# Performance work log

Hardware: AMD Instinct MI355X
Metric: run time of the kernel (lower is better)

## Reference

```python
import jax, jax.numpy as jnp
import numpy as np

B, S, D_MODEL = 2, 2048, 1024
N_HEADS, D_HEAD = 16, 64
ATTN_SCALE = float(np.sqrt(D_HEAD))
IGNORE = -100000.0


def setup_inputs() -> dict:
    key = jax.random.key(0)
    ks = jax.random.split(key, 8)
    scale = 1.0 / np.sqrt(D_MODEL)
    return {
        "x": jax.random.normal(ks[0], (B, S, D_MODEL), jnp.float32),
        "pos_embed": jax.random.normal(ks[1], (B, S, D_MODEL), jnp.float32),
        "W_Q": jax.random.normal(ks[2], (N_HEADS, D_MODEL, D_HEAD), jnp.float32) * scale,
        "b_Q": jnp.zeros((N_HEADS, D_HEAD), jnp.float32),
        "W_K": jax.random.normal(ks[3], (N_HEADS, D_MODEL, D_HEAD), jnp.float32) * scale,
        "b_K": jnp.zeros((N_HEADS, D_HEAD), jnp.float32),
        "W_V": jax.random.normal(ks[4], (N_HEADS, D_MODEL, D_HEAD), jnp.float32) * scale,
        "b_V": jnp.zeros((N_HEADS, D_HEAD), jnp.float32),
        "W_O": jax.random.normal(ks[5], (N_HEADS, D_HEAD, D_MODEL), jnp.float32) * (1.0 / np.sqrt(D_HEAD)),
        "b_O": jnp.zeros((D_MODEL,), jnp.float32),
    }


def reference(x, pos_embed, W_Q, b_Q, W_K, b_K, W_V, b_V, W_O, b_O):
    # use_pos_resid=False: q,k read x+pos_embed, v reads x
    attn_input = x + pos_embed                                   # [b,p,m]
    q = jnp.einsum('bpm,imh->bpih', attn_input, W_Q) + b_Q       # [b,p,i,h]
    k = jnp.einsum('bpm,imh->bpih', attn_input, W_K) + b_K
    v = jnp.einsum('bpm,imh->bpih', x, W_V) + b_V
    # scores[b,i,p,q]: query index p attends to key index q
    scores = jnp.einsum('bpih,bqih->bipq', q, k) / ATTN_SCALE
    S_len = scores.shape[-1]
    causal = jnp.tril(jnp.ones((S_len, S_len), bool))
    scores = jnp.where(causal, scores, IGNORE)
    attn = jax.nn.softmax(scores, axis=-1)                       # [b,i,q_dst,p_src]
    z = jnp.einsum('bpih,biqp->bqih', v, attn)                   # [b,q,i,h]
    out = jnp.einsum('bqih,ihm->bqm', z, W_O) + b_O              # [b,q,m]
    return out
```

## Files before the change

### kernel.cpp

```cpp
#include <hip/hip_runtime.h>
#include <hip/hip_bf16.h>
#include <stdint.h>

typedef __hip_bfloat16 bf16;
typedef __attribute__((ext_vector_type(8))) short short8;
typedef __attribute__((ext_vector_type(4))) short short4v;
typedef __attribute__((ext_vector_type(4))) float f32x4;
typedef __attribute__((ext_vector_type(16))) float f32x16;
typedef __attribute__((ext_vector_type(4))) unsigned uint4v;
typedef __attribute__((ext_vector_type(2))) unsigned uint2v;

#define AS1 __attribute__((address_space(1)))
#define AS3 __attribute__((address_space(3)))

static constexpr int SEQ = 2048, DM = 1024, DHD = 64;
static constexpr int MROWS = 2 * SEQ;

__device__ __forceinline__ short f2b(float f) {
  __hip_bfloat16 h = __float2bfloat16(f);
  return *reinterpret_cast<short*>(&h);
}

__device__ __forceinline__ unsigned pack2(float lo, float hi) {
  float2 fv; fv.x = lo; fv.y = hi;
  union { __hip_bfloat162 h; unsigned u; } cv;
  cv.h = __float22bfloat162_rn(fv);
  return cv.u;
}

__device__ __forceinline__ float fexp2(float x) {
#if __has_builtin(__builtin_amdgcn_exp2f)
  return __builtin_amdgcn_exp2f(x);
#else
  return exp2f(x);
#endif
}

union U8 { uint4v u; short8 s; };

#define GL16(dst, ptr, off) \
  asm volatile("global_load_dwordx4 %0, %1, off offset:" #off : "=v"(dst) : "v"(ptr))
#define WAITV(n) do { asm volatile("s_waitcnt vmcnt(" #n ")"); __builtin_amdgcn_sched_barrier(0); } while (0)

__device__ __forceinline__ float xmax32(float v) {
#if __has_builtin(__builtin_amdgcn_permlane32_swap)
  uint2v r = __builtin_amdgcn_permlane32_swap(__float_as_uint(v), __float_as_uint(v), false, false);
  return fmaxf(__uint_as_float(r[0]), __uint_as_float(r[1]));
#else
  return fmaxf(v, __shfl_xor(v, 32));
#endif
}
__device__ __forceinline__ float xsum32(float v) {
#if __has_builtin(__builtin_amdgcn_permlane32_swap)
  uint2v r = __builtin_amdgcn_permlane32_swap(__float_as_uint(v), __float_as_uint(v), false, false);
  return __uint_as_float(r[0]) + __uint_as_float(r[1]);
#else
  return v + __shfl_xor(v, 32);
#endif
}

__global__ __launch_bounds__(256) void preprocess(const float* __restrict__ x,
                                                  const float* __restrict__ pos,
                                                  bf16* __restrict__ xb,
                                                  bf16* __restrict__ aib,
                                                  const float* __restrict__ wq,
                                                  const float* __restrict__ wk,
                                                  const float* __restrict__ wv,
                                                  const float* __restrict__ wo,
                                                  bf16* __restrict__ oq,
                                                  bf16* __restrict__ ok,
                                                  bf16* __restrict__ ov,
                                                  bf16* __restrict__ owo) {
  const int bid = blockIdx.x;
  if (bid < 4096) {
    int i = bid * 256 + threadIdx.x;
    f32x4 xv = ((const f32x4*)x)[i];
    f32x4 pv = ((const f32x4*)pos)[i];
    short4v xo, ao;
#pragma unroll
    for (int j = 0; j < 4; ++j) {
      xo[j] = f2b(xv[j]);
      ao[j] = f2b(xv[j] + pv[j]);
    }
    ((short4v*)xb)[i] = xo;
    ((short4v*)aib)[i] = ao;
    return;
  }
  __shared__ float t[64][65];
  const float* in;
  bf16* out;
  int C, rt, ct;
  if (bid < 4864) {
    int idx = bid - 4096;
    int z = idx >> 4;
    rt = idx & 15; ct = 0; C = 64;
    const float* w = (z < 16) ? wq : (z < 32) ? wk : wv;
    bf16* o = (z < 16) ? oq : (z < 32) ? ok : ov;
    int zz = z & 15;
    in = w + (size_t)zz * 1024 * 64;
    out = o + (size_t)zz * 1024 * 64;
  } else {
    int idx = bid - 4864;
    ct = idx & 15; rt = idx >> 4; C = 1024;
    in = wo; out = owo;
  }
  int c = threadIdx.x & 63, g = threadIdx.x >> 6;
#pragma unroll
  for (int j = 0; j < 16; ++j) {
    int r = g * 16 + j;
    t[r][c] = in[(size_t)(rt * 64 + r) * C + (ct * 64 + c)];
  }
  __syncthreads();
#pragma unroll
  for (int j = 0; j < 16; ++j) {
    int rr = g * 16 + j;
    out[(size_t)(ct * 64 + rr) * 1024 + (rt * 64 + c)] = __float2bfloat16(t[c][rr]);
  }
}

template <int MODE>
__device__ __forceinline__ void gemm128_body(const bf16* __restrict__ A,
                                             const bf16* __restrict__ Bt,
                                             const float* __restrict__ bias,
                                             bf16* __restrict__ C, int mt, int nt,
                                             float scale) {
  __shared__ alignas(16) bf16 Al[128 * 32];
  __shared__ alignas(16) bf16 Bl[128 * 32];
  const int lane = threadIdx.x & 63, wv = threadIdx.x >> 6;
  const int wr = wv >> 1, wc = wv & 1;
  const bf16* Ab = A + (size_t)mt * 128 * DM;
  const bf16* Bb = Bt + (size_t)nt * 128 * DM;

  f32x4 acc[4][4];
#pragma unroll
  for (int i = 0; i < 4; ++i)
#pragma unroll
    for (int j = 0; j < 4; ++j) acc[i][j] = (f32x4){0.f, 0.f, 0.f, 0.f};

  for (int kt = 0; kt < DM / 32; ++kt) {
    int k0 = kt * 32;
#pragma unroll
    for (int c = 0; c < 2; ++c) {
      int li0 = wv * 64 + c * 256;
      int li = li0 + lane;
      int row = li >> 2, sl = li & 3;
      int gs = sl ^ ((row >> 1) & 3);
      __builtin_amdgcn_global_load_lds((const AS1 void*)(Ab + (size_t)row * DM + k0 + gs * 8),
                                       (AS3 void*)(&Al[li0 * 8]), 16, 0, 0);
    }
#pragma unroll
    for (int c = 0; c < 2; ++c) {
      int li0 = wv * 64 + c * 256;
      int li = li0 + lane;
      int row = li >> 2, sl = li & 3;
      int gs = sl ^ ((row >> 1) & 3);
      __builtin_amdgcn_global_load_lds((const AS1 void*)(Bb + (size_t)row * DM + k0 + gs * 8),
                                       (AS3 void*)(&Bl[li0 * 8]), 16, 0, 0);
    }
    __syncthreads();

    short8 af[4], bfr[4];
    const int kb = lane >> 4;
#pragma unroll
    for (int mi = 0; mi < 4; ++mi) {
      int r = wr * 64 + mi * 16 + (lane & 15);
      af[mi] = *(const short8*)(&Al[r * 32 + ((kb ^ ((r >> 1) & 3)) << 3)]);
    }
#pragma unroll
    for (int ni = 0; ni < 4; ++ni) {
      int r = wc * 64 + ni * 16 + (lane & 15);
      bfr[ni] = *(const short8*)(&Bl[r * 32 + ((kb ^ ((r >> 1) & 3)) << 3)]);
    }
#pragma unroll
    for (int mi = 0; mi < 4; ++mi)
#pragma unroll
      for (int ni = 0; ni < 4; ++ni)
        acc[mi][ni] = __builtin_amdgcn_mfma_f32_16x16x32_bf16(af[mi], bfr[ni], acc[mi][ni], 0, 0, 0);
    __syncthreads();
  }

#pragma unroll
  for (int mi = 0; mi < 4; ++mi) {
#pragma unroll
    for (int ni = 0; ni < 4; ++ni) {
      int row0 = mt * 128 + wr * 64 + mi * 16 + (lane >> 4) * 4;
      int col = nt * 128 + wc * 64 + ni * 16 + (lane & 15);
      float bv = bias[col];
      int bb = row0 >> 11, s0 = row0 & 2047;
      int hh = col >> 6, d0 = col & 63;
      size_t bhb = (size_t)(bb * 16 + hh) * 131072;
      if constexpr (MODE == 3) {
        int kc = d0 >> 4, hi = (d0 >> 3) & 1, e = d0 & 7;
        int g = s0 >> 5, r0 = s0 & 31;
        size_t bbase = bhb + g * 2048 + kc * 512 + e;
#pragma unroll
        for (int j = 0; j < 4; ++j)
          C[bbase + (size_t)(r0 + j + 32 * hi) * 8] =
              __float2bfloat16((acc[mi][ni][j] + bv) * scale);
      } else {
        int dj = d0 >> 5, d32 = d0 & 31;
        int ks = s0 >> 4, hi2 = (s0 >> 3) & 1, e0 = s0 & 7;
        short4v o;
#pragma unroll
        for (int j = 0; j < 4; ++j) o[j] = f2b(acc[mi][ni][j] + bv);
        *(short4v*)(C + bhb + dj * 65536 + ks * 512 + (size_t)(d32 + 32 * hi2) * 8 + e0) = o;
      }
    }
  }
}

static constexpr float QSCALE = 0.125f * 1.4426950408889634f;

__global__ __launch_bounds__(256) void qkv_gemm(const bf16* __restrict__ aib,
                                                const bf16* __restrict__ xb,
                                                const bf16* __restrict__ wqt,
                                                const bf16* __restrict__ wkt,
                                                const bf16* __restrict__ wvt,
                                                const float* __restrict__ bq,
                                                const float* __restrict__ bk,
                                                const float* __restrict__ bv,
                                                bf16* __restrict__ FQ, bf16* __restrict__ FK,
                                                bf16* __restrict__ FV) {
  int mt = blockIdx.x & 31;
  int nt = (blockIdx.x >> 5) & 7;
  int mat = blockIdx.x >> 8;
  if (mat == 0) {
    gemm128_body<3>(aib, wqt, bq, FQ, mt, nt, QSCALE);
  } else if (mat == 1) {
    gemm128_body<3>(aib, wkt, bk, FK, mt, nt, 1.0f);
  } else {
    gemm128_body<4>(xb, wvt, bv, FV, mt, nt, 1.0f);
  }
}

__global__ __launch_bounds__(256) void o_gemm64(const bf16* __restrict__ A,
                                                const bf16* __restrict__ Bt,
                                                const float* __restrict__ bias,
                                                float* __restrict__ out) {
  __shared__ alignas(16) bf16 Al[64 * 128];
  __shared__ alignas(16) bf16 Bl[128 * 128];
  const int mt = blockIdx.x & 63, nt = blockIdx.x >> 6;
  const int lane = threadIdx.x & 63, wv = threadIdx.x >> 6;
  const int wr = wv >> 1, wc = wv & 1;
  const bf16* Ab = A + (size_t)mt * 64 * DM;
  const bf16* Bb = Bt + (size_t)nt * 128 * DM;

  f32x4 acc[2][4];
#pragma unroll
  for (int i = 0; i < 2; ++i)
#pragma unroll
    for (int j = 0; j < 4; ++j) acc[i][j] = (f32x4){0.f, 0.f, 0.f, 0.f};

  for (int kt = 0; kt < DM / 128; ++kt) {
    int k0 = kt * 128;
#pragma unroll
    for (int c = 0; c < 4; ++c) {
      int li0 = wv * 64 + c * 256;
      int li = li0 + lane;
      int row = li >> 4, sl = li & 15;
      int gs = sl ^ (row & 7);
      __builtin_amdgcn_global_load_lds((const AS1 void*)(Ab + (size_t)row * DM + k0 + gs * 8),
                                       (AS3 void*)(&Al[li0 * 8]), 16, 0, 0);
    }
#pragma unroll
    for (int c = 0; c < 8; ++c) {
      int li0 = wv * 64 + c * 256;
      int li = li0 + lane;
      int row = li >> 4, sl = li & 15;
      int gs = sl ^ (row & 7);
      __builtin_amdgcn_global_load_lds((const AS1 void*)(Bb + (size_t)row * DM + k0 + gs * 8),
                                       (AS3 void*)(&Bl[li0 * 8]), 16, 0, 0);
    }
    __syncthreads();

    const int kb = lane >> 4;
#pragma unroll
    for (int kk = 0; kk < 4; ++kk) {
      short8 af[2], bfr[4];
#pragma unroll
      for (int mi = 0; mi < 2; ++mi) {
        int r = wr * 32 + mi * 16 + (lane & 15);
        af[mi] = *(const short8*)(&Al[r * 128 + (((kb + 4 * kk) ^ (r & 7)) << 3)]);
      }
#pragma unroll
      for (int ni = 0; ni < 4; ++ni) {
        int r = wc * 64 + ni * 16 + (lane & 15);
        bfr[ni] = *(const short8*)(&Bl[r * 128 + (((kb + 4 * kk) ^ (r & 7)) << 3)]);
      }
#pragma unroll
      for (int mi = 0; mi < 2; ++mi)
#pragma unroll
        for (int ni = 0; ni < 4; ++ni)
          acc[mi][ni] = __builtin_amdgcn_mfma_f32_16x16x32_bf16(af[mi], bfr[ni], acc[mi][ni], 0, 0, 0);
    }
    __syncthreads();
  }

#pragma unroll
  for (int mi = 0; mi < 2; ++mi) {
#pragma unroll
    for (int ni = 0; ni < 4; ++ni) {
      int row0 = mt * 64 + wr * 32 + mi * 16 + (lane >> 4) * 4;
      int col = nt * 128 + wc * 64 + ni * 16 + (lane & 15);
      float bv = bias[col];
#pragma unroll
      for (int j = 0; j < 4; ++j)
        out[(size_t)(row0 + j) * DM + col] = acc[mi][ni][j] + bv;
    }
  }
}

__global__ __launch_bounds__(128, 2) void flash_attn(const bf16* __restrict__ FQ,
                                                     const bf16* __restrict__ FK,
                                                     const bf16* __restrict__ FV,
                                                     bf16* __restrict__ Zb) {
  __shared__ float Zm[64][33];
  __shared__ float Ml[64], Ll[64];
  __shared__ unsigned Zl[32 * 32];

  const int lane = threadIdx.x & 63;
  const int wvi = threadIdx.x >> 6;
  const int qln = lane & 31;
  const bool hib = lane >= 32;
  const int bh = blockIdx.x & 31;
  const int wq = 63 - (blockIdx.x >> 5);
  const int bb = bh >> 4, h = bh & 15;
  const int q0 = wq * 32;
  const int nt = wq / 2 + 1;
  const int hsp = (nt + 1) >> 1;
  const int t0 = wvi ? hsp : 0;
  const int t1 = wvi ? nt : hsp;

  const size_t fb = (size_t)bh * 131072;
  const bf16* qp = FQ + fb + wq * 2048 + lane * 8;
  const bf16* kpt = FK + fb + (size_t)t0 * 4096 + lane * 8;
  const bf16* vp0 = FV + fb + (size_t)t0 * 2048 + lane * 8;
  const bf16* vp1 = vp0 + 65536;

  f32x16 zacc[2];
#pragma unroll
  for (int i = 0; i < 16; ++i) { zacc[0][i] = 0.f; zacc[1][i] = 0.f; }
  float mrun = -1e30f, lrun = 0.f;

  short8 qf[4];
  short8 kfA[2][4], kfB[2][4];
  short8 vf[2][4];

  if (t0 < t1) {
    GL16(qf[0], qp, 0); GL16(qf[1], qp, 1024); GL16(qf[2], qp, 2048); GL16(qf[3], qp, 3072);
    {
      const bf16* k1 = kpt + 2048;
      GL16(kfA[0][0], kpt, 0); GL16(kfA[0][1], kpt, 1024); GL16(kfA[0][2], kpt, 2048); GL16(kfA[0][3], kpt, 3072);
      GL16(kfA[1][0], k1, 0);  GL16(kfA[1][1], k1, 1024);  GL16(kfA[1][2], k1, 2048);  GL16(kfA[1][3], k1, 3072);
      kpt += 4096;
    }
    GL16(vf[0][0], vp0, 0); GL16(vf[0][1], vp0, 1024); GL16(vf[0][2], vp0, 2048); GL16(vf[0][3], vp0, 3072);
    GL16(vf[1][0], vp1, 0); GL16(vf[1][1], vp1, 1024); GL16(vf[1][2], vp1, 2048); GL16(vf[1][3], vp1, 3072);
    vp0 += 2048; vp1 += 2048;

    auto computeT = [&](short8(&kf)[2][4], short8(&kfn)[2][4], int t) {
      const int kv0 = t * 64;
      const bool pref = (t + 1 < t1);

      WAITV(8);

      f32x16 s[2];
#pragma unroll
      for (int i = 0; i < 16; ++i) { s[0][i] = 0.f; s[1][i] = 0.f; }
      __builtin_amdgcn_s_setprio(1);
#pragma unroll
      for (int kc = 0; kc < 4; ++kc) {
        s[0] = __builtin_amdgcn_mfma_f32_32x32x16_bf16(kf[0][kc], qf[kc], s[0], 0, 0, 0);
        s[1] = __builtin_amdgcn_mfma_f32_32x32x16_bf16(kf[1][kc], qf[kc], s[1], 0, 0, 0);
      }
      __builtin_amdgcn_s_setprio(0);

      if (pref) {
        const bf16* k1 = kpt + 2048;
        GL16(kfn[0][0], kpt, 0); GL16(kfn[0][1], kpt, 1024); GL16(kfn[0][2], kpt, 2048); GL16(kfn[0][3], kpt, 3072);
        GL16(kfn[1][0], k1, 0);  GL16(kfn[1][1], k1, 1024);  GL16(kfn[1][2], k1, 2048);  GL16(kfn[1][3], k1, 3072);
        kpt += 4096;
      }

      if (t == nt - 1) {
        const int qg = q0 + qln;
#pragma unroll
        for (int ni = 0; ni < 2; ++ni)
#pragma unroll
          for (int rr = 0; rr < 16; ++rr) {
            int kv = kv0 + 32 * ni + (rr & 3) + 8 * (rr >> 2) + (hib ? 4 : 0);
            if (kv > qg) s[ni][rr] = -1e30f;
          }
      }

      float t8[8];
#pragma unroll
      for (int i = 0; i < 8; ++i)
        t8[i] = fmaxf(fmaxf(s[0][i], s[0][i + 8]), fmaxf(s[1][i], s[1][i + 8]));
      float tm = fmaxf(fmaxf(fmaxf(t8[0], t8[1]), fmaxf(t8[2], t8[3])),
                       fmaxf(fmaxf(t8[4], t8[5]), fmaxf(t8[6], t8[7])));
      tm = xmax32(tm);

      if (__ballot(tm > mrun + 8.0f)) {
        float mn = fmaxf(mrun, tm);
        float al = fexp2(mrun - mn);
        mrun = mn;
        lrun *= al;
#pragma unroll
        for (int i = 0; i < 16; ++i) { zacc[0][i] *= al; zacc[1][i] *= al; }
      }

      float pacc[4] = {0.f, 0.f, 0.f, 0.f};
#pragma unroll
      for (int ni = 0; ni < 2; ++ni)
#pragma unroll
        for (int rr = 0; rr < 16; ++rr) {
          float p = fexp2(s[ni][rr] - mrun);
          s[ni][rr] = p;
          pacc[rr & 3] += p;
        }
      lrun += xsum32((pacc[0] + pacc[1]) + (pacc[2] + pacc[3]));

      unsigned su32[2][8];
#pragma unroll
      for (int ni = 0; ni < 2; ++ni)
#pragma unroll
        for (int tt = 0; tt < 8; ++tt)
          su32[ni][tt] = pack2(s[ni][2 * tt], s[ni][2 * tt + 1]);

      short8 pa[4];
#if __has_builtin(__builtin_amdgcn_permlane32_swap)
#pragma unroll
      for (int c = 0; c < 4; ++c) {
        int ni = c >> 1, b4 = 4 * (c & 1);
        uint2v r0 = __builtin_amdgcn_permlane32_swap(su32[ni][b4 + 0], su32[ni][b4 + 2], false, false);
        uint2v r1 = __builtin_amdgcn_permlane32_swap(su32[ni][b4 + 1], su32[ni][b4 + 3], false, false);
        U8 w;
        w.u[0] = r0[0]; w.u[1] = r1[0]; w.u[2] = r0[1]; w.u[3] = r1[1];
        pa[c] = w.s;
      }
#else
      unsigned X[2][8];
#pragma unroll
      for (int ni = 0; ni < 2; ++ni)
#pragma unroll
        for (int tt = 0; tt < 8; ++tt)
          X[ni][tt] = (unsigned)__shfl_xor((int)su32[ni][tt], 32);
#pragma unroll
      for (int c = 0; c < 4; ++c) {
        int ni = c >> 1, b4 = 4 * (c & 1);
        U8 w;
        w.u[0] = hib ? X[ni][b4 + 2] : su32[ni][b4 + 0];
        w.u[1] = hib ? X[ni][b4 + 3] : su32[ni][b4 + 1];
        w.u[2] = hib ? su32[ni][b4 + 2] : X[ni][b4 + 0];
        w.u[3] = hib ? su32[ni][b4 + 3] : X[ni][b4 + 1];
        pa[c] = w.s;
      }
#endif

      if (pref) { WAITV(8); } else { WAITV(0); }

      __builtin_amdgcn_s_setprio(1);
#pragma unroll
      for (int c = 0; c < 4; ++c) {
        zacc[0] = __builtin_amdgcn_mfma_f32_32x32x16_bf16(vf[0][c], pa[c], zacc[0], 0, 0, 0);
        zacc[1] = __builtin_amdgcn_mfma_f32_32x32x16_bf16(vf[1][c], pa[c], zacc[1], 0, 0, 0);
      }
      __builtin_amdgcn_s_setprio(0);
      __builtin_amdgcn_sched_barrier(0);

      if (pref) {
        GL16(vf[0][0], vp0, 0); GL16(vf[0][1], vp0, 1024); GL16(vf[0][2], vp0, 2048); GL16(vf[0][3], vp0, 3072);
        GL16(vf[1][0], vp1, 0); GL16(vf[1][1], vp1, 1024); GL16(vf[1][2], vp1, 2048); GL16(vf[1][3], vp1, 3072);
        vp0 += 2048; vp1 += 2048;
      }
    };

    int t = t0;
    while (true) {
      computeT(kfA, kfB, t);
      if (++t >= t1) break;
      computeT(kfB, kfA, t);
      if (++t >= t1) break;
    }
  }

  if (wvi == 1) {
#pragma unroll
    for (int i = 0; i < 16; ++i) {
      Zm[lane][i] = zacc[0][i];
      Zm[lane][16 + i] = zacc[1][i];
    }
    Ml[lane] = mrun;
    Ll[lane] = lrun;
  }
  __syncthreads();
  if (wvi == 0) {
    float m1 = Ml[lane], l1 = Ll[lane];
    float mn = fmaxf(mrun, m1);
    float a0 = fexp2(mrun - mn);
    float a1 = fexp2(m1 - mn);
    float lm = lrun * a0 + l1 * a1;
#pragma unroll
    for (int i = 0; i < 16; ++i) {
      zacc[0][i] = zacc[0][i] * a0 + Zm[lane][i] * a1;
      zacc[1][i] = zacc[1][i] * a0 + Zm[lane][16 + i] * a1;
    }

    const float rl = 1.0f / lm;
    const int W8[8] = {0, 1, 4, 5, 8, 9, 12, 13};
#pragma unroll
    for (int dj = 0; dj < 2; ++dj)
#pragma unroll
      for (int tt = 0; tt < 8; ++tt) {
        unsigned v = pack2(zacc[dj][2 * tt] * rl, zacc[dj][2 * tt + 1] * rl);
        int x = 16 * dj + (hib ? 2 : 0) + W8[tt];
        Zl[qln * 32 + (((x >> 2) ^ (qln & 7)) << 2) + (x & 3)] = v;
      }
    asm volatile("s_waitcnt lgkmcnt(0)" ::: "memory");
    __builtin_amdgcn_sched_barrier(0);
    const size_t base = ((size_t)bb * SEQ) * DM + h * DHD;
    int q2 = lane >> 1, hf = lane & 1;
#pragma unroll
    for (int u = 0; u < 4; ++u) {
      int sl = (hf * 4 + u) ^ (q2 & 7);
      U8 w;
      w.u = *(const uint4v*)&Zl[q2 * 32 + sl * 4];
      *(short8*)(Zb + base + (size_t)(q0 + q2) * DM + hf * 32 + u * 8) = w.s;
    }
  }
}

extern "C" void kernel_launch(void* const* d_in, const int* in_sizes, int n_in,
                              void* d_out, int out_size, void* d_ws, size_t ws_size,
                              hipStream_t stream) {
  (void)in_sizes; (void)n_in; (void)out_size; (void)ws_size;
  const float* x = (const float*)d_in[0];
  const float* pos = (const float*)d_in[1];
  const float* WQ = (const float*)d_in[2];
  const float* bQ = (const float*)d_in[3];
  const float* WK = (const float*)d_in[4];
  const float* bK = (const float*)d_in[5];
  const float* WV = (const float*)d_in[6];
  const float* bV = (const float*)d_in[7];
  const float* WO = (const float*)d_in[8];
  const float* bO = (const float*)d_in[9];
  float* out = (float*)d_out;

  bf16* ws = (bf16*)d_ws;
  size_t off = 0;
  bf16* aib = ws + off; off += (size_t)MROWS * DM;
  bf16* xb  = ws + off; off += (size_t)MROWS * DM;
  bf16* wqt = ws + off; off += (size_t)DM * DM;
  bf16* wkt = ws + off; off += (size_t)DM * DM;
  bf16* wvt = ws + off; off += (size_t)DM * DM;
  bf16* wot = ws + off; off += (size_t)DM * DM;
  bf16* FQ  = ws + off; off += (size_t)MROWS * DM;
  bf16* FK  = ws + off; off += (size_t)MROWS * DM;
  bf16* FV  = ws + off; off += (size_t)MROWS * DM;
  bf16* Zb  = ws + off; off += (size_t)MROWS * DM;

  preprocess<<<5120, 256, 0, stream>>>(x, pos, xb, aib, WQ, WK, WV, WO,
                                       wqt, wkt, wvt, wot);
  qkv_gemm<<<768, 256, 0, stream>>>(aib, xb, wqt, wkt, wvt, bQ, bK, bV, FQ, FK, FV);
  flash_attn<<<2048, 128, 0, stream>>>(FQ, FK, FV, Zb);
  o_gemm64<<<512, 256, 0, stream>>>(Zb, wot, bO, out);
}
```

Baseline: 103.6 us.

## Pair long and short causal query tiles per block to balance attention work

Each flash-attention block now handles two query tiles, a long one (63-p) and a short one (p), instead of one. The work of both is split between the two waves: wave 0 runs the first part of the long tile, and wave 1 runs the rest of the long tile followed by the whole short tile. The long tile's two partial softmax states are merged through shared memory, and each wave writes out one tile. This halves the grid and evens out causal-triangle work across blocks, meant to cut tail imbalance. The cost is fewer blocks for latency hiding and serial segments inside wave 1.

```diff
diff --git a/kernel.cpp b/kernel.cpp
--- a/kernel.cpp
+++ b/kernel.cpp
@@ -316,37 +316,155 @@
                                                      bf16* __restrict__ Zb) {
   __shared__ float Zm[64][33];
   __shared__ float Ml[64], Ll[64];
-  __shared__ unsigned Zl[32 * 32];
+  __shared__ unsigned Zl[2][32 * 32];
 
   const int lane = threadIdx.x & 63;
   const int wvi = threadIdx.x >> 6;
   const int qln = lane & 31;
   const bool hib = lane >= 32;
   const int bh = blockIdx.x & 31;
-  const int wq = 63 - (blockIdx.x >> 5);
-  const int bb = bh >> 4, h = bh & 15;
-  const int q0 = wq * 32;
-  const int nt = wq / 2 + 1;
-  const int hsp = (nt + 1) >> 1;
-  const int t0 = wvi ? hsp : 0;
-  const int t1 = wvi ? nt : hsp;
-
+  const int p = blockIdx.x >> 5;
+  const int wqA = 63 - p, wqB = p;
+  const int nA = wqA / 2 + 1, nB = wqB / 2 + 1;
+  int h = (nA + nB + 1) >> 1;
+  if (h > nA) h = nA;
+  const int bb = bh >> 4, hd = bh & 15;
   const size_t fb = (size_t)bh * 131072;
-  const bf16* qp = FQ + fb + wq * 2048 + lane * 8;
-  const bf16* kpt = FK + fb + (size_t)t0 * 4096 + lane * 8;
-  const bf16* vp0 = FV + fb + (size_t)t0 * 2048 + lane * 8;
-  const bf16* vp1 = vp0 + 65536;
+  const size_t base = ((size_t)bb * SEQ) * DM + hd * DHD;
 
   f32x16 zacc[2];
-#pragma unroll
-  for (int i = 0; i < 16; ++i) { zacc[0][i] = 0.f; zacc[1][i] = 0.f; }
-  float mrun = -1e30f, lrun = 0.f;
-
+  float mrun, lrun;
   short8 qf[4];
   short8 kfA[2][4], kfB[2][4];
   short8 vf[2][4];
 
-  if (t0 < t1) {
+  auto computeT = [&](short8(&kf)[2][4], short8(&kfn)[2][4], int t, int q0,
+                      int ntq, int te, const bf16*& kpt, const bf16*& vp0,
+                      const bf16*& vp1) {
+    const int kv0 = t * 64;
+    const bool pref = (t + 1 < te);
+
+    WAITV(8);
+
+    f32x16 s[2];
+#pragma unroll
+    for (int i = 0; i < 16; ++i) { s[0][i] = 0.f; s[1][i] = 0.f; }
+    __builtin_amdgcn_s_setprio(1);
+#pragma unroll
+    for (int kc = 0; kc < 4; ++kc) {
+      s[0] = __builtin_amdgcn_mfma_f32_32x32x16_bf16(kf[0][kc], qf[kc], s[0], 0, 0, 0);
+      s[1] = __builtin_amdgcn_mfma_f32_32x32x16_bf16(kf[1][kc], qf[kc], s[1], 0, 0, 0);
+    }
+    __builtin_amdgcn_s_setprio(0);
+
+    if (pref) {
+      const bf16* k1 = kpt + 2048;
+      GL16(kfn[0][0], kpt, 0); GL16(kfn[0][1], kpt, 1024); GL16(kfn[0][2], kpt, 2048); GL16(kfn[0][3], kpt, 3072);
+      GL16(kfn[1][0], k1, 0);  GL16(kfn[1][1], k1, 1024);  GL16(kfn[1][2], k1, 2048);  GL16(kfn[1][3], k1, 3072);
+      kpt += 4096;
+    }
+
+    if (t == ntq - 1) {
+      const int qg = q0 + qln;
+#pragma unroll
+      for (int ni = 0; ni < 2; ++ni)
+#pragma unroll
+        for (int rr = 0; rr < 16; ++rr) {
+          int kv = kv0 + 32 * ni + (rr & 3) + 8 * (rr >> 2) + (hib ? 4 : 0);
+          if (kv > qg) s[ni][rr] = -1e30f;
+        }
+    }
+
+    float t8[8];
+#pragma unroll
+    for (int i = 0; i < 8; ++i)
+      t8[i] = fmaxf(fmaxf(s[0][i], s[0][i + 8]), fmaxf(s[1][i], s[1][i + 8]));
+    float tm = fmaxf(fmaxf(fmaxf(t8[0], t8[1]), fmaxf(t8[2], t8[3])),
+                     fmaxf(fmaxf(t8[4], t8[5]), fmaxf(t8[6], t8[7])));
+    tm = xmax32(tm);
+
+    if (__ballot(tm > mrun + 8.0f)) {
+      float mn = fmaxf(mrun, tm);
+      float al = fexp2(mrun - mn);
+      mrun = mn;
+      lrun *= al;
+#pragma unroll
+      for (int i = 0; i < 16; ++i) { zacc[0][i] *= al; zacc[1][i] *= al; }
+    }
+
+    float pacc[4] = {0.f, 0.f, 0.f, 0.f};
+#pragma unroll
+    for (int ni = 0; ni < 2; ++ni)
+#pragma unroll
+      for (int rr = 0; rr < 16; ++rr) {
+        float pw = fexp2(s[ni][rr] - mrun);
+        s[ni][rr] = pw;
+        pacc[rr & 3] += pw;
+      }
+    lrun += xsum32((pacc[0] + pacc[1]) + (pacc[2] + pacc[3]));
+
+    unsigned su32[2][8];
+#pragma unroll
+    for (int ni = 0; ni < 2; ++ni)
+#pragma unroll
+      for (int tt = 0; tt < 8; ++tt)
+        su32[ni][tt] = pack2(s[ni][2 * tt], s[ni][2 * tt + 1]);
+
+    short8 pa[4];
+#if __has_builtin(__builtin_amdgcn_permlane32_swap)
+#pragma unroll
+    for (int c = 0; c < 4; ++c) {
+      int ni = c >> 1, b4 = 4 * (c & 1);
+      uint2v r0 = __builtin_amdgcn_permlane32_swap(su32[ni][b4 + 0], su32[ni][b4 + 2], false, false);
+      uint2v r1 = __builtin_amdgcn_permlane32_swap(su32[ni][b4 + 1], su32[ni][b4 + 3], false, false);
+      U8 w;
+      w.u[0] = r0[0]; w.u[1] = r1[0]; w.u[2] = r0[1]; w.u[3] = r1[1];
+      pa[c] = w.s;
+    }
+#else
+    unsigned X[2][8];
+#pragma unroll
+    for (int ni = 0; ni < 2; ++ni)
+#pragma unroll
+      for (int tt = 0; tt < 8; ++tt)
+        X[ni][tt] = (unsigned)__shfl_xor((int)su32[ni][tt], 32);
+#pragma unroll
+    for (int c = 0; c < 4; ++c) {
+      int ni = c >> 1, b4 = 4 * (c & 1);
+      U8 w;
+      w.u[0] = hib ? X[ni][b4 + 2] : su32[ni][b4 + 0];
+      w.u[1] = hib ? X[ni][b4 + 3] : su32[ni][b4 + 1];
+      w.u[2] = hib ? su32[ni][b4 + 2] : X[ni][b4 + 0];
+      w.u[3] = hib ? su32[ni][b4 + 3] : X[ni][b4 + 1];
+      pa[c] = w.s;
+    }
+#endif
+
+    if (pref) { WAITV(8); } else { WAITV(0); }
+
+    __builtin_amdgcn_s_setprio(1);
+#pragma unroll
+    for (int c = 0; c < 4; ++c) {
+      zacc[0] = __builtin_amdgcn_mfma_f32_32x32x16_bf16(vf[0][c], pa[c], zacc[0], 0, 0, 0);
+      zacc[1] = __builtin_amdgcn_mfma_f32_32x32x16_bf16(vf[1][c], pa[c], zacc[1], 0, 0, 0);
+    }
+    __builtin_amdgcn_s_setprio(0);
+    __builtin_amdgcn_sched_barrier(0);
+
+    if (pref) {
+      GL16(vf[0][0], vp0, 0); GL16(vf[0][1], vp0, 1024); GL16(vf[0][2], vp0, 2048); GL16(vf[0][3], vp0, 3072);
+      GL16(vf[1][0], vp1, 0); GL16(vf[1][1], vp1, 1024); GL16(vf[1][2], vp1, 2048); GL16(vf[1][3], vp1, 3072);
+      vp0 += 2048; vp1 += 2048;
+    }
+  };
+
+  auto runSeg = [&](int qt, int ntq, int ts, int te) {
+    if (ts >= te) return;
+    const int q0 = qt * 32;
+    const bf16* qp = FQ + fb + qt * 2048 + lane * 8;
+    const bf16* kpt = FK + fb + (size_t)ts * 4096 + lane * 8;
+    const bf16* vp0 = FV + fb + (size_t)ts * 2048 + lane * 8;
+    const bf16* vp1 = vp0 + 65536;
     GL16(qf[0], qp, 0); GL16(qf[1], qp, 1024); GL16(qf[2], qp, 2048); GL16(qf[3], qp, 3072);
     {
       const bf16* k1 = kpt + 2048;
@@ -358,134 +476,50 @@
     GL16(vf[1][0], vp1, 0); GL16(vf[1][1], vp1, 1024); GL16(vf[1][2], vp1, 2048); GL16(vf[1][3], vp1, 3072);
     vp0 += 2048; vp1 += 2048;
 
-    auto computeT = [&](short8(&kf)[2][4], short8(&kfn)[2][4], int t) {
-      const int kv0 = t * 64;
-      const bool pref = (t + 1 < t1);
-
-      WAITV(8);
-
-      f32x16 s[2];
-#pragma unroll
-      for (int i = 0; i < 16; ++i) { s[0][i] = 0.f; s[1][i] = 0.f; }
-      __builtin_amdgcn_s_setprio(1);
-#pragma unroll
-      for (int kc = 0; kc < 4; ++kc) {
-        s[0] = __builtin_amdgcn_mfma_f32_32x32x16_bf16(kf[0][kc], qf[kc], s[0], 0, 0, 0);
-        s[1] = __builtin_amdgcn_mfma_f32_32x32x16_bf16(kf[1][kc], qf[kc], s[1], 0, 0, 0);
+    int t = ts;
+    while (true) {
+      computeT(kfA, kfB, t, q0, ntq, te, kpt, vp0, vp1);
+      if (++t >= te) break;
+      computeT(kfB, kfA, t, q0, ntq, te, kpt, vp0, vp1);
+      if (++t >= te) break;
+    }
+  };
+
+  auto resetState = [&]() {
+#pragma unroll
+    for (int i = 0; i < 16; ++i) { zacc[0][i] = 0.f; zacc[1][i] = 0.f; }
+    mrun = -1e30f; lrun = 0.f;
+  };
+
+  auto writeOut = [&](int qt, float lm, unsigned* Zbuf) {
+    const float rl = 1.0f / lm;
+    const int W8[8] = {0, 1, 4, 5, 8, 9, 12, 13};
+#pragma unroll
+    for (int dj = 0; dj < 2; ++dj)
+#pragma unroll
+      for (int tt = 0; tt < 8; ++tt) {
+        unsigned v = pack2(zacc[dj][2 * tt] * rl, zacc[dj][2 * tt + 1] * rl);
+        int x = 16 * dj + (hib ? 2 : 0) + W8[tt];
+        Zbuf[qln * 32 + (((x >> 2) ^ (qln & 7)) << 2) + (x & 3)] = v;
       }
-      __builtin_amdgcn_s_setprio(0);
-
-      if (pref) {
-        const bf16* k1 = kpt + 2048;
-        GL16(kfn[0][0], kpt, 0); GL16(kfn[0][1], kpt, 1024); GL16(kfn[0][2], kpt, 2048); GL16(kfn[0][3], kpt, 3072);
-        GL16(kfn[1][0], k1, 0);  GL16(kfn[1][1], k1, 1024);  GL16(kfn[1][2], k1, 2048);  GL16(kfn[1][3], k1, 3072);
-        kpt += 4096;
-      }
-
-      if (t == nt - 1) {
-        const int qg = q0 + qln;
-#pragma unroll
-        for (int ni = 0; ni < 2; ++ni)
-#pragma unroll
-          for (int rr = 0; rr < 16; ++rr) {
-            int kv = kv0 + 32 * ni + (rr & 3) + 8 * (rr >> 2) + (hib ? 4 : 0);
-            if (kv > qg) s[ni][rr] = -1e30f;
-          }
-      }
-
-      float t8[8];
-#pragma unroll
-      for (int i = 0; i < 8; ++i)
-        t8[i] = fmaxf(fmaxf(s[0][i], s[0][i + 8]), fmaxf(s[1][i], s[1][i + 8]));
-      float tm = fmaxf(fmaxf(fmaxf(t8[0], t8[1]), fmaxf(t8[2], t8[3])),
-                       fmaxf(fmaxf(t8[4], t8[5]), fmaxf(t8[6], t8[7])));
-      tm = xmax32(tm);
-
-      if (__ballot(tm > mrun + 8.0f)) {
-        float mn = fmaxf(mrun, tm);
-        float al = fexp2(mrun - mn);
-        mrun = mn;
-        lrun *= al;
-#pragma unroll
-        for (int i = 0; i < 16; ++i) { zacc[0][i] *= al; zacc[1][i] *= al; }
-      }
-
-      float pacc[4] = {0.f, 0.f, 0.f, 0.f};
-#pragma unroll
-      for (int ni = 0; ni < 2; ++ni)
-#pragma unroll
-        for (int rr = 0; rr < 16; ++rr) {
-          float p = fexp2(s[ni][rr] - mrun);
-          s[ni][rr] = p;
-          pacc[rr & 3] += p;
-        }
-      lrun += xsum32((pacc[0] + pacc[1]) + (pacc[2] + pacc[3]));
-
-      unsigned su32[2][8];
-#pragma unroll
-      for (int ni = 0; ni < 2; ++ni)
-#pragma unroll
-        for (int tt = 0; tt < 8; ++tt)
-          su32[ni][tt] = pack2(s[ni][2 * tt], s[ni][2 * tt + 1]);
-
-      short8 pa[4];
-#if __has_builtin(__builtin_amdgcn_permlane32_swap)
-#pragma unroll
-      for (int c = 0; c < 4; ++c) {
-        int ni = c >> 1, b4 = 4 * (c & 1);
-        uint2v r0 = __builtin_amdgcn_permlane32_swap(su32[ni][b4 + 0], su32[ni][b4 + 2], false, false);
-        uint2v r1 = __builtin_amdgcn_permlane32_swap(su32[ni][b4 + 1], su32[ni][b4 + 3], false, false);
-        U8 w;
-        w.u[0] = r0[0]; w.u[1] = r1[0]; w.u[2] = r0[1]; w.u[3] = r1[1];
-        pa[c] = w.s;
-      }
-#else
-      unsigned X[2][8];
-#pragma unroll
-      for (int ni = 0; ni < 2; ++ni)
-#pragma unroll
-        for (int tt = 0; tt < 8; ++tt)
-          X[ni][tt] = (unsigned)__shfl_xor((int)su32[ni][tt], 32);
-#pragma unroll
-      for (int c = 0; c < 4; ++c) {
-        int ni = c >> 1, b4 = 4 * (c & 1);
-        U8 w;
-        w.u[0] = hib ? X[ni][b4 + 2] : su32[ni][b4 + 0];
-        w.u[1] = hib ? X[ni][b4 + 3] : su32[ni][b4 + 1];
-        w.u[2] = hib ? su32[ni][b4 + 2] : X[ni][b4 + 0];
-        w.u[3] = hib ? su32[ni][b4 + 3] : X[ni][b4 + 1];
-        pa[c] = w.s;
-      }
-#endif
-
-      if (pref) { WAITV(8); } else { WAITV(0); }
-
-      __builtin_amdgcn_s_setprio(1);
-#pragma unroll
-      for (int c = 0; c < 4; ++c) {
-        zacc[0] = __builtin_amdgcn_mfma_f32_32x32x16_bf16(vf[0][c], pa[c], zacc[0], 0, 0, 0);
-        zacc[1] = __builtin_amdgcn_mfma_f32_32x32x16_bf16(vf[1][c], pa[c], zacc[1], 0, 0, 0);
-      }
-      __builtin_amdgcn_s_setprio(0);
-      __builtin_amdgcn_sched_barrier(0);
-
-      if (pref) {
-        GL16(vf[0][0], vp0, 0); GL16(vf[0][1], vp0, 1024); GL16(vf[0][2], vp0, 2048); GL16(vf[0][3], vp0, 3072);
-        GL16(vf[1][0], vp1, 0); GL16(vf[1][1], vp1, 1024); GL16(vf[1][2], vp1, 2048); GL16(vf[1][3], vp1, 3072);
-        vp0 += 2048; vp1 += 2048;
-      }
-    };
-
-    int t = t0;
-    while (true) {
-      computeT(kfA, kfB, t);
-      if (++t >= t1) break;
-      computeT(kfB, kfA, t);
-      if (++t >= t1) break;
-    }
-  }
-
-  if (wvi == 1) {
+    asm volatile("s_waitcnt lgkmcnt(0)" ::: "memory");
+    __builtin_amdgcn_sched_barrier(0);
+    int q2 = lane >> 1, hf = lane & 1;
+#pragma unroll
+    for (int u = 0; u < 4; ++u) {
+      int sl = (hf * 4 + u) ^ (q2 & 7);
+      U8 w;
+      w.u = *(const uint4v*)&Zbuf[q2 * 32 + sl * 4];
+      *(short8*)(Zb + base + (size_t)(qt * 32 + q2) * DM + hf * 32 + u * 8) = w.s;
+    }
+  };
+
+  if (wvi == 0) {
+    resetState();
+    runSeg(wqA, nA, 0, h);
+  } else {
+    resetState();
+    runSeg(wqA, nA, h, nA);
 #pragma unroll
     for (int i = 0; i < 16; ++i) {
       Zm[lane][i] = zacc[0][i];
@@ -493,8 +527,11 @@
     }
     Ml[lane] = mrun;
     Ll[lane] = lrun;
+    resetState();
+    runSeg(wqB, nB, 0, nB);
   }
   __syncthreads();
+
   if (wvi == 0) {
     float m1 = Ml[lane], l1 = Ll[lane];
     float mn = fmaxf(mrun, m1);
@@ -506,28 +543,9 @@
       zacc[0][i] = zacc[0][i] * a0 + Zm[lane][i] * a1;
       zacc[1][i] = zacc[1][i] * a0 + Zm[lane][16 + i] * a1;
     }
-
-    const float rl = 1.0f / lm;
-    const int W8[8] = {0, 1, 4, 5, 8, 9, 12, 13};
-#pragma unroll
-    for (int dj = 0; dj < 2; ++dj)
-#pragma unroll
-      for (int tt = 0; tt < 8; ++tt) {
-        unsigned v = pack2(zacc[dj][2 * tt] * rl, zacc[dj][2 * tt + 1] * rl);
-        int x = 16 * dj + (hib ? 2 : 0) + W8[tt];
-        Zl[qln * 32 + (((x >> 2) ^ (qln & 7)) << 2) + (x & 3)] = v;
-      }
-    asm volatile("s_waitcnt lgkmcnt(0)" ::: "memory");
-    __builtin_amdgcn_sched_barrier(0);
-    const size_t base = ((size_t)bb * SEQ) * DM + h * DHD;
-    int q2 = lane >> 1, hf = lane & 1;
-#pragma unroll
-    for (int u = 0; u < 4; ++u) {
-      int sl = (hf * 4 + u) ^ (q2 & 7);
-      U8 w;
-      w.u = *(const uint4v*)&Zl[q2 * 32 + sl * 4];
-      *(short8*)(Zb + base + (size_t)(q0 + q2) * DM + hf * 32 + u * 8) = w.s;
-    }
+    writeOut(wqA, lm, Zl[0]);
+  } else {
+    writeOut(wqB, lrun, Zl[1]);
   }
 }
 
@@ -563,6 +581,6 @@
   preprocess<<<5120, 256, 0, stream>>>(x, pos, xb, aib, WQ, WK, WV, WO,
                                        wqt, wkt, wvt, wot);
   qkv_gemm<<<768, 256, 0, stream>>>(aib, xb, wqt, wkt, wvt, bQ, bK, bV, FQ, FK, FV);
-  flash_attn<<<2048, 128, 0, stream>>>(FQ, FK, FV, Zb);
+  flash_attn<<<1024, 128, 0, stream>>>(FQ, FK, FV, Zb);
   o_gemm64<<<512, 256, 0, stream>>>(Zb, wot, bO, out);
 }
```

After: 99.56 us (median of 3 runs). -3.9%, faster.
